# Kernel tuning notes

Measured on AMD Instinct MI355X. Metric: run time of the kernel, lower is better.

The kernel has to match this reference:

```python
import jax, jax.numpy as jnp
import numpy as np
import math

EMBED = 256
NH = 8      # num_heads
NP = 4      # num_points
HD = EMBED // NH  # head_dim = 32
BS = 8
NQ = 8192
HH = 128
WW = 128


def setup_inputs() -> dict:
    key = jax.random.key(0)
    ks = jax.random.split(key, 12)
    query = jax.random.normal(ks[0], (BS, NQ, EMBED), jnp.float32)
    reference_points = jax.random.uniform(ks[1], (BS, NQ, 2), dtype=jnp.float32)
    value = jax.random.normal(ks[2], (BS, HH * WW, EMBED), jnp.float32)
    # sampling_offsets: torch init uses zero weight + structured bias (rose pattern);
    # use small random weight so the math path is exercised, keep the structured bias.
    w_off = 0.001 * jax.random.normal(ks[3], (EMBED, NH * NP * 2), jnp.float32)
    thetas = np.arange(NH, dtype=np.float32) * (2.0 * math.pi / NH)
    grid = np.stack([np.cos(thetas), np.sin(thetas)], -1)          # [NH, 2]
    grid = np.tile(grid[:, None, :], (1, NP, 1)) * np.arange(1, NP + 1, dtype=np.float32)[None, :, None]
    b_off = jnp.asarray(grid.reshape(-1), jnp.float32)              # [NH*NP*2]
    w_attn = 0.01 * jax.random.normal(ks[4], (EMBED, NH * NP), jnp.float32)
    b_attn = jnp.zeros((NH * NP,), jnp.float32)
    xav = 1.0 / math.sqrt(EMBED)
    w_val = xav * jax.random.normal(ks[5], (EMBED, EMBED), jnp.float32)
    b_val = jnp.zeros((EMBED,), jnp.float32)
    w_out = xav * jax.random.normal(ks[6], (EMBED, EMBED), jnp.float32)
    b_out = jnp.zeros((EMBED,), jnp.float32)
    return {"query": query, "reference_points": reference_points, "value": value,
            "w_off": w_off, "b_off": b_off, "w_attn": w_attn, "b_attn": b_attn,
            "w_val": w_val, "b_val": b_val, "w_out": w_out, "b_out": b_out,
            "H": HH, "W": WW}


def _deform_attn(query, reference_points, value, w_off, b_off, w_attn, b_attn,
                 w_val, b_val, w_out, b_out, H, W):
    bs, nq, _ = query.shape
    # value projection -> [bs, nh, H*W, hd]
    v = (value @ w_val + b_val).reshape(bs, H * W, NH, HD).transpose(0, 2, 1, 3)
    # offsets and attention weights
    off = (query @ w_off + b_off).reshape(bs, nq, NH, NP, 2)
    attn = jax.nn.softmax((query @ w_attn + b_attn).reshape(bs, nq, NH, NP), axis=-1)
    norm = jnp.array([W, H], dtype=query.dtype)
    loc = reference_points[:, :, None, None, :] + off / norm       # [bs,nq,nh,np,2] in [0,1]
    # grid_sample, align_corners=False: pixel = loc*size - 0.5  (x <-> W, y <-> H)
    px = (loc[..., 0] * W - 0.5).transpose(0, 2, 1, 3).reshape(bs, NH, nq * NP)
    py = (loc[..., 1] * H - 0.5).transpose(0, 2, 1, 3).reshape(bs, NH, nq * NP)
    x0 = jnp.floor(px); y0 = jnp.floor(py)
    wx = px - x0; wy = py - y0
    x0i = x0.astype(jnp.int32); y0i = y0.astype(jnp.int32)

    def gather(xi, yi):
        # padding_mode='zeros': out-of-range corners contribute 0
        mask = ((xi >= 0) & (xi < W) & (yi >= 0) & (yi < H)).astype(v.dtype)
        idx = jnp.clip(yi, 0, H - 1) * W + jnp.clip(xi, 0, W - 1)   # [bs,nh,K]
        g = jnp.take_along_axis(v, idx[..., None], axis=2)          # [bs,nh,K,hd]
        return g * mask[..., None]

    samp = (((1 - wx) * (1 - wy))[..., None] * gather(x0i, y0i)
            + (wx * (1 - wy))[..., None] * gather(x0i + 1, y0i)
            + ((1 - wx) * wy)[..., None] * gather(x0i, y0i + 1)
            + (wx * wy)[..., None] * gather(x0i + 1, y0i + 1))      # [bs,nh,nq*np,hd]
    samp = samp.reshape(bs, NH, nq, NP, HD)
    aw = attn.transpose(0, 2, 1, 3)                                 # [bs,nh,nq,np]
    out = jnp.einsum('bhqpd,bhqp->bqhd', samp, aw).reshape(bs, nq, EMBED)
    return out @ w_out + b_out


def reference(query, reference_points, value, w_off, b_off, w_attn, b_attn,
              w_val, b_val, w_out, b_out, H, W):
    return _deform_attn(query, reference_points, value, w_off, b_off, w_attn, b_attn,
                        w_val, b_val, w_out, b_out, H, W)
```

## Files before the change

### kernel.cpp

```cpp
#include <hip/hip_runtime.h>
#include <stdint.h>

#define NQ 8192
#define BSZ 8
#define NH 8
#define NP 4
#define HD 32
#define EMBED 256
#define IMG 128
#define NPIX (IMG*IMG)

typedef __attribute__((ext_vector_type(8))) short short8v;
typedef __attribute__((ext_vector_type(4))) float f32x4;

static __device__ __forceinline__ float bf2f(uint32_t u) {
    union { uint32_t i; float f; } x; x.i = u << 16; return x.f;
}
static __device__ __forceinline__ uint16_t f2bf(float f) {
    union { float f; uint32_t i; } x; x.f = f;
    uint32_t r = x.i + 0x7fffu + ((x.i >> 16) & 1u);
    return (uint16_t)(r >> 16);
}
static __device__ __forceinline__ uint32_t cvtpk(float lo, float hi) {
    uint32_t r;
    asm("v_cvt_pk_bf16_f32 %0, %1, %2" : "=v"(r) : "v"(lo), "v"(hi));
    return r;
}
static __device__ __forceinline__ void gload_lds16(const void* g, void* l) {
    __builtin_amdgcn_global_load_lds(
        (const __attribute__((address_space(1))) unsigned int*)g,
        (__attribute__((address_space(3))) unsigned int*)l, 16, 0, 0);
}

#define WAITV(n)   asm volatile("s_waitcnt vmcnt(" #n ")" ::: "memory")
#define WAITLGKM() asm volatile("s_waitcnt lgkmcnt(0)" ::: "memory")
#define BAR()      __builtin_amdgcn_s_barrier()
#define CLOBBER()  asm volatile("" ::: "memory")

static __device__ __forceinline__ void waitv_n(int n) {
    switch (n) {
        case 0: WAITV(0); break;  case 1: WAITV(1); break;
        case 2: WAITV(2); break;  case 3: WAITV(3); break;
        case 4: WAITV(4); break;  case 5: WAITV(5); break;
        case 6: WAITV(6); break;  case 7: WAITV(7); break;
        case 8: WAITV(8); break;  default: WAITV(10); break;
    }
}

__global__ void pack_w(const float* __restrict__ w_val, const float* __restrict__ w_out,
                       const float* __restrict__ w_off, const float* __restrict__ w_attn,
                       uint16_t* __restrict__ wTval, uint16_t* __restrict__ wTout,
                       uint16_t* __restrict__ wTcat) {
    int k = blockIdx.x;
    int n = threadIdx.x;
    wTval[n * 256 + k] = f2bf(w_val[k * 256 + n]);
    wTout[n * 256 + k] = f2bf(w_out[k * 256 + n]);
    if (n < 64)       wTcat[n * 256 + k]        = f2bf(w_off[k * 64 + n]);
    else if (n < 96)  wTcat[n * 256 + k]        = f2bf(w_attn[k * 32 + (n - 64)]);
}

__global__ __launch_bounds__(512, 2)
void vproj4(const float* __restrict__ Ap, const uint16_t* __restrict__ BT,
            uint16_t* __restrict__ Vp, const float* __restrict__ bias) {
    __shared__ char SMEM[73728];
    char* ring = SMEM;
    char* Cs = SMEM + 65536;
    const int tid = threadIdx.x, w = tid >> 6, l = tid & 63;
    const int bid = blockIdx.x;
    const int row0 = bid * 256;

    auto stageA = [&](int t) {
        const int gr0 = row0 + t * 16;
#pragma unroll
        for (int c = 0; c < 2; ++c) {
            int loff = c * 8192 + tid * 16;
            int row = loff >> 10, x = loff & 1023;
            const char* src = (const char*)Ap + (size_t)(gr0 + row) * 1024
                              + (x ^ ((row & 7) << 4));
            gload_lds16(src, ring + (t & 3) * 16384 + c * 8192 + w * 1024);
        }
    };

    short8v breg[2][8];
    float bv[2];
#pragma unroll
    for (int n = 0; n < 2; ++n) {
        int col = w * 32 + n * 16 + (l & 15);
        bv[n] = bias[col];
        const char* bb = (const char*)BT + (size_t)col * 512 + (l >> 4) * 16;
#pragma unroll
        for (int k = 0; k < 8; ++k)
            breg[n][k] = *(const short8v*)(bb + k * 64);
    }

    stageA(0); stageA(1); stageA(2);

    for (int t = 0; t < 16; ++t) {
        int nw;
        if (t == 0) nw = 4;
        else if (t == 1) nw = 5;
        else if (t == 2) nw = 6;
        else if (t <= 13) nw = 7;
        else if (t == 14) nw = 5;
        else nw = 3;
        waitv_n(nw);
        BAR(); CLOBBER();
        if (t + 3 < 16) stageA(t + 3);

        const char* base = ring + (t & 3) * 16384 + (l & 15) * 1024;
        const int sz = (l & 7) << 4;
        short8v a[8];
#pragma unroll
        for (int k = 0; k < 8; ++k) {
            int off = k * 128 + (l >> 4) * 32;
            f32x4 lo = *(const f32x4*)(base + (off ^ sz));
            f32x4 hi = *(const f32x4*)(base + ((off + 16) ^ sz));
            union { uint32_t u[4]; short8v s8; } pk;
            pk.u[0] = cvtpk(lo[0], lo[1]); pk.u[1] = cvtpk(lo[2], lo[3]);
            pk.u[2] = cvtpk(hi[0], hi[1]); pk.u[3] = cvtpk(hi[2], hi[3]);
            a[k] = pk.s8;
        }
        f32x4 acc[2] = {};
#pragma unroll
        for (int k = 0; k < 8; ++k)
#pragma unroll
            for (int n = 0; n < 2; ++n)
                acc[n] = __builtin_amdgcn_mfma_f32_16x16x32_bf16(a[k], breg[n][k], acc[n], 0, 0, 0);

        const int gr0 = row0 + t * 16;
#pragma unroll
        for (int n = 0; n < 2; ++n) {
            int lcol = w * 32 + n * 16 + (l & 15);
#pragma unroll
            for (int r = 0; r < 4; ++r) {
                int lrow = (l >> 4) * 4 + r;
                *(uint16_t*)(Cs + ((lrow * 512 + lcol * 2) ^ ((lrow & 7) << 4)))
                    = f2bf(acc[n][r] + bv[n]);
            }
        }
        WAITLGKM();
        BAR(); CLOBBER();
        const int b_ = gr0 >> 14, pix0 = gr0 & 16383;
        {
            int fb = l * 16;
            int lrow = fb >> 6, dbyte = fb & 63;
            uint4 d = *(const uint4*)(Cs + ((lrow * 512 + w * 64 + dbyte)
                                            ^ ((lrow & 7) << 4)));
            *(uint4*)((char*)Vp + (((size_t)(b_ * 8 + w)) << 20)
                      + (size_t)(pix0 + lrow) * 64 + dbyte) = d;
        }
    }
}

template<int STRIPES>
__global__ __launch_bounds__(512, 2)
void gemm_pk(const void* __restrict__ Ap, const uint16_t* __restrict__ BT,
             void* __restrict__ Cp, const float* __restrict__ bias) {
    constexpr int NR = 16;
    constexpr int T  = STRIPES * 4;
    __shared__ char SMEM[131072];
    char* ring = SMEM;
    const int tid = threadIdx.x, w = tid >> 6, l = tid & 63;
    const int stripe0 = blockIdx.x * STRIPES;

    auto stageA = [&](int slot, int t) {
        const int gr0 = (stripe0 + (t >> 2)) * 64 + (t & 3) * 16;
        int loff = tid * 16;
        int row = loff >> 9, x = loff & 511;
        const char* src = (const char*)Ap + (size_t)(gr0 + row) * 512
                          + (x ^ ((row & 7) << 4));
        gload_lds16(src, ring + slot * 8192 + w * 1024);
    };

#pragma unroll
    for (int c = 0; c < 16; ++c) {
        int loff = c * 8192 + tid * 16;
        int row = loff >> 9, x = loff & 511;
        const char* src = (const char*)BT + (size_t)row * 512 + (x ^ ((row & 7) << 4));
        gload_lds16(src, SMEM + c * 8192 + w * 1024);
    }
    WAITV(0);
    BAR();
    CLOBBER();
    short8v breg[2][8];
#pragma unroll
    for (int n = 0; n < 2; ++n) {
        int col = w * 32 + n * 16 + (l & 15);
        const char* base = SMEM + col * 512;
        const int sz = (col & 7) << 4;
#pragma unroll
        for (int k = 0; k < 8; ++k)
            breg[n][k] = *(const short8v*)(base + ((k * 64 + (l >> 4) * 16) ^ sz));
    }
    WAITLGKM();
    BAR();
    CLOBBER();
#pragma unroll
    for (int t = 0; t < 6; ++t) stageA(t & (NR - 1), t);

    for (int st = 0; st < STRIPES; ++st) {
        f32x4 acc[4][2] = {};
#pragma unroll
        for (int s = 0; s < 4; ++s) {
            const int t = st * 4 + s;
            const int rem = T - 1 - t;
            waitv_n(rem < 5 ? rem : 5);
            BAR();
            CLOBBER();
            if (t + 6 < T) stageA((t + 6) & (NR - 1), t + 6);
            const int slot = t & (NR - 1);
            short8v a[8];
            const int sz = (l & 7) << 4;
            const char* base = ring + slot * 8192 + (l & 15) * 512;
#pragma unroll
            for (int k = 0; k < 8; ++k)
                a[k] = *(const short8v*)(base + ((k * 64 + (l >> 4) * 16) ^ sz));
#pragma unroll
            for (int k = 0; k < 8; ++k)
#pragma unroll
                for (int n = 0; n < 2; ++n)
                    acc[s][n] = __builtin_amdgcn_mfma_f32_16x16x32_bf16(a[k], breg[n][k], acc[s][n], 0, 0, 0);
        }
        const int gr0 = (stripe0 + st) * 64;
#pragma unroll
        for (int s = 0; s < 4; ++s)
#pragma unroll
            for (int n = 0; n < 2; ++n) {
                int col = w * 32 + n * 16 + (l & 15);
                float bv = bias[col];
#pragma unroll
                for (int r = 0; r < 4; ++r) {
                    int gr = gr0 + s * 16 + (l >> 4) * 4 + r;
                    ((float*)Cp)[(size_t)gr * 256 + col] = acc[s][n][r] + bv;
                }
            }
    }
}

__global__ __launch_bounds__(256, 2)
void proj_kernel(const float* __restrict__ Q, const uint16_t* __restrict__ WTcat,
                 const float* __restrict__ b_off, const float* __restrict__ b_attn,
                 const float* __restrict__ refp,
                 float* __restrict__ locs, float* __restrict__ attnw) {
    __shared__ uint16_t Bs[96 * 256];
    __shared__ uint16_t As[64 * 256];
    const int tid = threadIdx.x, w = tid >> 6, l = tid & 63;
    const int blk = blockIdx.x;

#pragma unroll
    for (int c = 0; c < 12; ++c) {
        int loff = (w * 12 + c) * 1024;
        int lofl = loff + l * 16;
        int row = lofl >> 9, colb = lofl & 511;
        const char* src = (const char*)WTcat + (size_t)row * 512 + (colb ^ ((row & 7) << 4));
        gload_lds16(src, (char*)Bs + loff);
    }
#pragma unroll
    for (int c = 0; c < 8; ++c) {
        int loff = tid * 16 + c * 4096;
        int row = loff >> 9, colb = loff & 511;
        const float* src = Q + (size_t)(blk * 64 + row) * 256 + (colb >> 1);
        float4 f0 = *(const float4*)src;
        float4 f1 = *(const float4*)(src + 4);
        uint4 pk;
        pk.x = (uint32_t)f2bf(f0.x) | ((uint32_t)f2bf(f0.y) << 16);
        pk.y = (uint32_t)f2bf(f0.z) | ((uint32_t)f2bf(f0.w) << 16);
        pk.z = (uint32_t)f2bf(f1.x) | ((uint32_t)f2bf(f1.y) << 16);
        pk.w = (uint32_t)f2bf(f1.z) | ((uint32_t)f2bf(f1.w) << 16);
        *(uint4*)((char*)As + row * 512 + (colb ^ ((row & 7) << 4))) = pk;
    }
    __syncthreads();

    f32x4 acc[6] = {};
    const int arow = w * 16 + (l & 15);
#pragma unroll
    for (int ks = 0; ks < 8; ++ks) {
        const int kb = ks * 64 + (l >> 4) * 16;
        short8v a = *(const short8v*)((const char*)As + arow * 512 + (kb ^ ((arow & 7) << 4)));
#pragma unroll
        for (int n = 0; n < 6; ++n) {
            int col = n * 16 + (l & 15);
            short8v b = *(const short8v*)((const char*)Bs + col * 512 + (kb ^ ((col & 7) << 4)));
            acc[n] = __builtin_amdgcn_mfma_f32_16x16x32_bf16(a, b, acc[n], 0, 0, 0);
        }
    }
    __syncthreads();
    float* scores = (float*)As;
#pragma unroll
    for (int n = 0; n < 6; ++n)
#pragma unroll
        for (int r = 0; r < 4; ++r)
            scores[(w * 16 + (l >> 4) * 4 + r) * 96 + n * 16 + (l & 15)] = acc[n][r];
    __syncthreads();

    for (int it = tid; it < 512; it += 256) {
        int row = it >> 3, h = it & 7;
        int gq = blk * 64 + row;
        int b = gq >> 13, q = gq & 8191;
        size_t itemH = ((size_t)(b * 8 + h) << 13) | q;
        float s0 = scores[row * 96 + 64 + h * 4 + 0] + b_attn[h * 4 + 0];
        float s1 = scores[row * 96 + 64 + h * 4 + 1] + b_attn[h * 4 + 1];
        float s2 = scores[row * 96 + 64 + h * 4 + 2] + b_attn[h * 4 + 2];
        float s3 = scores[row * 96 + 64 + h * 4 + 3] + b_attn[h * 4 + 3];
        float mx = fmaxf(fmaxf(s0, s1), fmaxf(s2, s3));
        float e0 = __expf(s0 - mx), e1 = __expf(s1 - mx);
        float e2 = __expf(s2 - mx), e3 = __expf(s3 - mx);
        float inv = 1.0f / (e0 + e1 + e2 + e3);
        float rx = refp[gq * 2 + 0] * 128.0f - 0.5f;
        float ry = refp[gq * 2 + 1] * 128.0f - 0.5f;
        float ew[4] = { e0, e1, e2, e3 };
#pragma unroll
        for (int p = 0; p < 4; ++p) {
            float ox = scores[row * 96 + h * 8 + p * 2 + 0] + b_off[h * 8 + p * 2 + 0];
            float oy = scores[row * 96 + h * 8 + p * 2 + 1] + b_off[h * 8 + p * 2 + 1];
            locs[itemH * 8 + p * 2 + 0] = rx + ox;
            locs[itemH * 8 + p * 2 + 1] = ry + oy;
            attnw[itemH * 4 + p] = ew[p] * inv;
        }
    }
}

__global__ __launch_bounds__(256)
void sample_kernel(const uint16_t* __restrict__ v, const float* __restrict__ locs,
                   const float* __restrict__ attnw, uint16_t* __restrict__ oatt) {
    const int bid = blockIdx.x;
    const int h = bid & 7;
    const int rest = bid >> 3;
    const int b = rest >> 7;
    const int chunk = rest & 127;
    const int qloc = threadIdx.x >> 2;
    const int dg = threadIdx.x & 3;
    const int q = chunk * 64 + qloc;
    const size_t itemH = ((size_t)(b * 8 + h) << 13) | q;
    const char* plane = (const char*)v + ((size_t)(b * 8 + h) << 20);

    float4 l01 = ((const float4*)locs)[itemH * 2 + 0];
    float4 l23 = ((const float4*)locs)[itemH * 2 + 1];
    float4 aw4 = ((const float4*)attnw)[itemH];
    float pxs[4] = { l01.x, l01.z, l23.x, l23.z };
    float pys[4] = { l01.y, l01.w, l23.y, l23.w };
    float aws[4] = { aw4.x, aw4.y, aw4.z, aw4.w };

    float acc[8] = {};
#pragma unroll
    for (int p = 0; p < 4; ++p) {
        float px = pxs[p], py = pys[p], aw = aws[p];
        float fx = floorf(px), fy = floorf(py);
        float wx = px - fx, wy = py - fy;
        int x0 = (int)fx, y0 = (int)fy;
#pragma unroll
        for (int cy = 0; cy < 2; ++cy) {
            int yy = y0 + cy;
            float wyv = cy ? wy : 1.f - wy;
            bool yok = (unsigned)yy < (unsigned)IMG;
            int yc = min(max(yy, 0), IMG - 1);
#pragma unroll
            for (int cx = 0; cx < 2; ++cx) {
                int xx = x0 + cx;
                bool ok = yok && ((unsigned)xx < (unsigned)IMG);
                int xc = min(max(xx, 0), IMG - 1);
                float wgt = ok ? aw * (cx ? wx : 1.f - wx) * wyv : 0.f;
                const uint4 u = *(const uint4*)(plane + ((size_t)(yc * IMG + xc) << 6) + dg * 16);
                acc[0] += wgt * bf2f(u.x & 0xffffu);
                acc[1] += wgt * bf2f(u.x >> 16);
                acc[2] += wgt * bf2f(u.y & 0xffffu);
                acc[3] += wgt * bf2f(u.y >> 16);
                acc[4] += wgt * bf2f(u.z & 0xffffu);
                acc[5] += wgt * bf2f(u.z >> 16);
                acc[6] += wgt * bf2f(u.w & 0xffffu);
                acc[7] += wgt * bf2f(u.w >> 16);
            }
        }
    }
    const size_t bq = (size_t)b * NQ + q;
    uint4 out;
    out.x = (uint32_t)f2bf(acc[0]) | ((uint32_t)f2bf(acc[1]) << 16);
    out.y = (uint32_t)f2bf(acc[2]) | ((uint32_t)f2bf(acc[3]) << 16);
    out.z = (uint32_t)f2bf(acc[4]) | ((uint32_t)f2bf(acc[5]) << 16);
    out.w = (uint32_t)f2bf(acc[6]) | ((uint32_t)f2bf(acc[7]) << 16);
    *(uint4*)((char*)oatt + (bq * 256 + h * 32 + dg * 8) * 2) = out;
}

extern "C" void kernel_launch(void* const* d_in, const int* in_sizes, int n_in,
                              void* d_out, int out_size, void* d_ws, size_t ws_size,
                              hipStream_t stream) {
    const float* query  = (const float*)d_in[0];
    const float* refp   = (const float*)d_in[1];
    const float* value  = (const float*)d_in[2];
    const float* w_off  = (const float*)d_in[3];
    const float* b_off  = (const float*)d_in[4];
    const float* w_attn = (const float*)d_in[5];
    const float* b_attn = (const float*)d_in[6];
    const float* w_val  = (const float*)d_in[7];
    const float* b_val  = (const float*)d_in[8];
    const float* w_out  = (const float*)d_in[9];
    const float* b_out  = (const float*)d_in[10];

    char* ws = (char*)d_ws;
    uint16_t* v     = (uint16_t*)(ws);
    uint16_t* oatt  = (uint16_t*)(ws + (64u << 20));
    float*    locs  = (float*)(ws + (96u << 20));
    float*    attnw = (float*)(ws + (112u << 20));
    uint16_t* wTval = (uint16_t*)(ws + (120u << 20));
    uint16_t* wTout = (uint16_t*)(ws + (120u << 20) + 131072);
    uint16_t* wTcat = (uint16_t*)(ws + (120u << 20) + 262144);

    pack_w<<<256, 256, 0, stream>>>(w_val, w_out, w_off, w_attn, wTval, wTout, wTcat);
    vproj4<<<512, 512, 0, stream>>>(value, wTval, v, b_val);
    proj_kernel<<<1024, 256, 0, stream>>>(query, wTcat, b_off, b_attn, refp, locs, attnw);
    sample_kernel<<<8192, 256, 0, stream>>>(v, locs, attnw, oatt);
    gemm_pk<4><<<256, 512, 0, stream>>>(oatt, wTout, (float*)d_out, b_out);
}
```

Before: 139.6 us.

## Fuse bilinear sampling with output projection GEMM in one kernel

Merges the sampling kernel and the output-projection GEMM into a single kernel. Each 512-thread block handles 64 queries across all 8 heads, writes the sampled bf16 tile into swizzled LDS, then runs MFMA against the output weights held in registers and writes fp32 output plus bias. This removes the global round trip of the intermediate attention tensor and one launch. The cost is that the weight fragments are loaded straight from global memory by every block, and the gather phase now overlaps less with the GEMM inside a block.

```diff
diff --git a/kernel.cpp b/kernel.cpp
--- a/kernel.cpp
+++ b/kernel.cpp
@@ -149,91 +149,6 @@
             *(uint4*)((char*)Vp + (((size_t)(b_ * 8 + w)) << 20)
                       + (size_t)(pix0 + lrow) * 64 + dbyte) = d;
         }
-    }
-}
-
-template<int STRIPES>
-__global__ __launch_bounds__(512, 2)
-void gemm_pk(const void* __restrict__ Ap, const uint16_t* __restrict__ BT,
-             void* __restrict__ Cp, const float* __restrict__ bias) {
-    constexpr int NR = 16;
-    constexpr int T  = STRIPES * 4;
-    __shared__ char SMEM[131072];
-    char* ring = SMEM;
-    const int tid = threadIdx.x, w = tid >> 6, l = tid & 63;
-    const int stripe0 = blockIdx.x * STRIPES;
-
-    auto stageA = [&](int slot, int t) {
-        const int gr0 = (stripe0 + (t >> 2)) * 64 + (t & 3) * 16;
-        int loff = tid * 16;
-        int row = loff >> 9, x = loff & 511;
-        const char* src = (const char*)Ap + (size_t)(gr0 + row) * 512
-                          + (x ^ ((row & 7) << 4));
-        gload_lds16(src, ring + slot * 8192 + w * 1024);
-    };
-
-#pragma unroll
-    for (int c = 0; c < 16; ++c) {
-        int loff = c * 8192 + tid * 16;
-        int row = loff >> 9, x = loff & 511;
-        const char* src = (const char*)BT + (size_t)row * 512 + (x ^ ((row & 7) << 4));
-        gload_lds16(src, SMEM + c * 8192 + w * 1024);
-    }
-    WAITV(0);
-    BAR();
-    CLOBBER();
-    short8v breg[2][8];
-#pragma unroll
-    for (int n = 0; n < 2; ++n) {
-        int col = w * 32 + n * 16 + (l & 15);
-        const char* base = SMEM + col * 512;
-        const int sz = (col & 7) << 4;
-#pragma unroll
-        for (int k = 0; k < 8; ++k)
-            breg[n][k] = *(const short8v*)(base + ((k * 64 + (l >> 4) * 16) ^ sz));
-    }
-    WAITLGKM();
-    BAR();
-    CLOBBER();
-#pragma unroll
-    for (int t = 0; t < 6; ++t) stageA(t & (NR - 1), t);
-
-    for (int st = 0; st < STRIPES; ++st) {
-        f32x4 acc[4][2] = {};
-#pragma unroll
-        for (int s = 0; s < 4; ++s) {
-            const int t = st * 4 + s;
-            const int rem = T - 1 - t;
-            waitv_n(rem < 5 ? rem : 5);
-            BAR();
-            CLOBBER();
-            if (t + 6 < T) stageA((t + 6) & (NR - 1), t + 6);
-            const int slot = t & (NR - 1);
-            short8v a[8];
-            const int sz = (l & 7) << 4;
-            const char* base = ring + slot * 8192 + (l & 15) * 512;
-#pragma unroll
-            for (int k = 0; k < 8; ++k)
-                a[k] = *(const short8v*)(base + ((k * 64 + (l >> 4) * 16) ^ sz));
-#pragma unroll
-            for (int k = 0; k < 8; ++k)
-#pragma unroll
-                for (int n = 0; n < 2; ++n)
-                    acc[s][n] = __builtin_amdgcn_mfma_f32_16x16x32_bf16(a[k], breg[n][k], acc[s][n], 0, 0, 0);
-        }
-        const int gr0 = (stripe0 + st) * 64;
-#pragma unroll
-        for (int s = 0; s < 4; ++s)
-#pragma unroll
-            for (int n = 0; n < 2; ++n) {
-                int col = w * 32 + n * 16 + (l & 15);
-                float bv = bias[col];
-#pragma unroll
-                for (int r = 0; r < 4; ++r) {
-                    int gr = gr0 + s * 16 + (l >> 4) * 4 + r;
-                    ((float*)Cp)[(size_t)gr * 256 + col] = acc[s][n][r] + bv;
-                }
-            }
     }
 }
 
@@ -320,65 +235,111 @@
     }
 }
 
-__global__ __launch_bounds__(256)
-void sample_kernel(const uint16_t* __restrict__ v, const float* __restrict__ locs,
-                   const float* __restrict__ attnw, uint16_t* __restrict__ oatt) {
+__global__ __launch_bounds__(512, 2)
+void samp_oproj(const uint16_t* __restrict__ v, const float* __restrict__ locs,
+                const float* __restrict__ attnw, const uint16_t* __restrict__ BT,
+                float* __restrict__ Out, const float* __restrict__ bias) {
+    __shared__ char Cs[32768];
+    const int tid = threadIdx.x, w = tid >> 6, l = tid & 63;
     const int bid = blockIdx.x;
-    const int h = bid & 7;
-    const int rest = bid >> 3;
-    const int b = rest >> 7;
-    const int chunk = rest & 127;
-    const int qloc = threadIdx.x >> 2;
-    const int dg = threadIdx.x & 3;
-    const int q = chunk * 64 + qloc;
-    const size_t itemH = ((size_t)(b * 8 + h) << 13) | q;
+    const int b = bid >> 7;
+    const int q0 = (bid & 127) * 64;
+    const int h = w;
+
+    short8v breg[2][8];
+    float bv[2];
+#pragma unroll
+    for (int n = 0; n < 2; ++n) {
+        int col = w * 32 + n * 16 + (l & 15);
+        bv[n] = bias[col];
+        const char* bb = (const char*)BT + (size_t)col * 512 + (l >> 4) * 16;
+#pragma unroll
+        for (int k = 0; k < 8; ++k)
+            breg[n][k] = *(const short8v*)(bb + k * 64);
+    }
+
     const char* plane = (const char*)v + ((size_t)(b * 8 + h) << 20);
-
-    float4 l01 = ((const float4*)locs)[itemH * 2 + 0];
-    float4 l23 = ((const float4*)locs)[itemH * 2 + 1];
-    float4 aw4 = ((const float4*)attnw)[itemH];
-    float pxs[4] = { l01.x, l01.z, l23.x, l23.z };
-    float pys[4] = { l01.y, l01.w, l23.y, l23.w };
-    float aws[4] = { aw4.x, aw4.y, aw4.z, aw4.w };
-
-    float acc[8] = {};
-#pragma unroll
-    for (int p = 0; p < 4; ++p) {
-        float px = pxs[p], py = pys[p], aw = aws[p];
-        float fx = floorf(px), fy = floorf(py);
-        float wx = px - fx, wy = py - fy;
-        int x0 = (int)fx, y0 = (int)fy;
-#pragma unroll
-        for (int cy = 0; cy < 2; ++cy) {
-            int yy = y0 + cy;
-            float wyv = cy ? wy : 1.f - wy;
-            bool yok = (unsigned)yy < (unsigned)IMG;
-            int yc = min(max(yy, 0), IMG - 1);
-#pragma unroll
-            for (int cx = 0; cx < 2; ++cx) {
-                int xx = x0 + cx;
-                bool ok = yok && ((unsigned)xx < (unsigned)IMG);
-                int xc = min(max(xx, 0), IMG - 1);
-                float wgt = ok ? aw * (cx ? wx : 1.f - wx) * wyv : 0.f;
-                const uint4 u = *(const uint4*)(plane + ((size_t)(yc * IMG + xc) << 6) + dg * 16);
-                acc[0] += wgt * bf2f(u.x & 0xffffu);
-                acc[1] += wgt * bf2f(u.x >> 16);
-                acc[2] += wgt * bf2f(u.y & 0xffffu);
-                acc[3] += wgt * bf2f(u.y >> 16);
-                acc[4] += wgt * bf2f(u.z & 0xffffu);
-                acc[5] += wgt * bf2f(u.z >> 16);
-                acc[6] += wgt * bf2f(u.w & 0xffffu);
-                acc[7] += wgt * bf2f(u.w >> 16);
+    const int dg = l & 3;
+#pragma unroll
+    for (int pass = 0; pass < 4; ++pass) {
+        const int qi = pass * 16 + (l >> 2);
+        const size_t itemH = ((size_t)(b * 8 + h) << 13) | (q0 + qi);
+        float4 l01 = ((const float4*)locs)[itemH * 2 + 0];
+        float4 l23 = ((const float4*)locs)[itemH * 2 + 1];
+        float4 aw4 = ((const float4*)attnw)[itemH];
+        float pxs[4] = { l01.x, l01.z, l23.x, l23.z };
+        float pys[4] = { l01.y, l01.w, l23.y, l23.w };
+        float aws[4] = { aw4.x, aw4.y, aw4.z, aw4.w };
+        float acc[8] = {};
+#pragma unroll
+        for (int p = 0; p < 4; ++p) {
+            float px = pxs[p], py = pys[p], aw = aws[p];
+            float fx = floorf(px), fy = floorf(py);
+            float wx = px - fx, wy = py - fy;
+            int x0 = (int)fx, y0 = (int)fy;
+#pragma unroll
+            for (int cy = 0; cy < 2; ++cy) {
+                int yy = y0 + cy;
+                float wyv = cy ? wy : 1.f - wy;
+                bool yok = (unsigned)yy < (unsigned)IMG;
+                int yc = min(max(yy, 0), IMG - 1);
+#pragma unroll
+                for (int cx = 0; cx < 2; ++cx) {
+                    int xx = x0 + cx;
+                    bool ok = yok && ((unsigned)xx < (unsigned)IMG);
+                    int xc = min(max(xx, 0), IMG - 1);
+                    float wgt = ok ? aw * (cx ? wx : 1.f - wx) * wyv : 0.f;
+                    const uint4 u = *(const uint4*)(plane
+                        + ((size_t)(yc * IMG + xc) << 6) + dg * 16);
+                    acc[0] += wgt * bf2f(u.x & 0xffffu);
+                    acc[1] += wgt * bf2f(u.x >> 16);
+                    acc[2] += wgt * bf2f(u.y & 0xffffu);
+                    acc[3] += wgt * bf2f(u.y >> 16);
+                    acc[4] += wgt * bf2f(u.z & 0xffffu);
+                    acc[5] += wgt * bf2f(u.z >> 16);
+                    acc[6] += wgt * bf2f(u.w & 0xffffu);
+                    acc[7] += wgt * bf2f(u.w >> 16);
+                }
             }
         }
-    }
-    const size_t bq = (size_t)b * NQ + q;
-    uint4 out;
-    out.x = (uint32_t)f2bf(acc[0]) | ((uint32_t)f2bf(acc[1]) << 16);
-    out.y = (uint32_t)f2bf(acc[2]) | ((uint32_t)f2bf(acc[3]) << 16);
-    out.z = (uint32_t)f2bf(acc[4]) | ((uint32_t)f2bf(acc[5]) << 16);
-    out.w = (uint32_t)f2bf(acc[6]) | ((uint32_t)f2bf(acc[7]) << 16);
-    *(uint4*)((char*)oatt + (bq * 256 + h * 32 + dg * 8) * 2) = out;
+        uint4 o;
+        o.x = (uint32_t)f2bf(acc[0]) | ((uint32_t)f2bf(acc[1]) << 16);
+        o.y = (uint32_t)f2bf(acc[2]) | ((uint32_t)f2bf(acc[3]) << 16);
+        o.z = (uint32_t)f2bf(acc[4]) | ((uint32_t)f2bf(acc[5]) << 16);
+        o.w = (uint32_t)f2bf(acc[6]) | ((uint32_t)f2bf(acc[7]) << 16);
+        *(uint4*)(Cs + ((qi * 512 + h * 64 + dg * 16) ^ ((qi & 7) << 4))) = o;
+    }
+    WAITLGKM();
+    BAR(); CLOBBER();
+
+    f32x4 acc2[4][2] = {};
+#pragma unroll
+    for (int m = 0; m < 4; ++m) {
+        const int row = m * 16 + (l & 15);
+        const char* base = Cs + row * 512;
+        const int sz = (row & 7) << 4;
+        short8v a[8];
+#pragma unroll
+        for (int k = 0; k < 8; ++k)
+            a[k] = *(const short8v*)(base + ((k * 64 + (l >> 4) * 16) ^ sz));
+#pragma unroll
+        for (int k = 0; k < 8; ++k)
+#pragma unroll
+            for (int n = 0; n < 2; ++n)
+                acc2[m][n] = __builtin_amdgcn_mfma_f32_16x16x32_bf16(a[k], breg[n][k], acc2[m][n], 0, 0, 0);
+    }
+    float* outb = Out + ((size_t)b * NQ + q0) * 256;
+#pragma unroll
+    for (int m = 0; m < 4; ++m)
+#pragma unroll
+        for (int n = 0; n < 2; ++n) {
+            int col = w * 32 + n * 16 + (l & 15);
+#pragma unroll
+            for (int r = 0; r < 4; ++r) {
+                int row = m * 16 + (l >> 4) * 4 + r;
+                outb[(size_t)row * 256 + col] = acc2[m][n][r] + bv[n];
+            }
+        }
 }
 
 extern "C" void kernel_launch(void* const* d_in, const int* in_sizes, int n_in,
@@ -398,7 +359,6 @@
 
     char* ws = (char*)d_ws;
     uint16_t* v     = (uint16_t*)(ws);
-    uint16_t* oatt  = (uint16_t*)(ws + (64u << 20));
     float*    locs  = (float*)(ws + (96u << 20));
     float*    attnw = (float*)(ws + (112u << 20));
     uint16_t* wTval = (uint16_t*)(ws + (120u << 20));
@@ -408,6 +368,5 @@
     pack_w<<<256, 256, 0, stream>>>(w_val, w_out, w_off, w_attn, wTval, wTout, wTcat);
     vproj4<<<512, 512, 0, stream>>>(value, wTval, v, b_val);
     proj_kernel<<<1024, 256, 0, stream>>>(query, wTcat, b_off, b_attn, refp, locs, attnw);
-    sample_kernel<<<8192, 256, 0, stream>>>(v, locs, attnw, oatt);
-    gemm_pk<4><<<256, 512, 0, stream>>>(oatt, wTout, (float*)d_out, b_out);
-}
+    samp_oproj<<<1024, 512, 0, stream>>>(v, locs, attnw, wTout, (float*)d_out, b_out);
+}
```

Measured after the change: 156.6 us. +12.2%, slower.
